# Performance work log

Hardware: AMD Instinct MI355X
Metric: run time of the kernel (lower is better)

The kernel has to match this reference:

```python
import math
import jax, jax.numpy as jnp
import numpy as np

NEG_BIG = -1e12  # matches torch's -1000000000000.0 padding


def setup_inputs() -> dict:
    key = jax.random.key(0)
    k1, k2, k3 = jax.random.split(key, 3)
    bs, n_tok, n_heads, width = 1, 4096, 8, 64
    dst_mxlen, src_mxlen = 32, 64
    q = jax.random.normal(k1, (bs, n_tok, n_heads, width), dtype=jnp.float32)
    k = jax.random.normal(k2, (bs, n_tok, n_heads, width), dtype=jnp.float32)
    v = jax.random.normal(k3, (bs, n_tok, n_heads, width), dtype=jnp.float32)
    # Sliding-window COO: each dst attends to its dst_mxlen preceding tokens (clipped).
    dst = jnp.repeat(jnp.arange(n_tok, dtype=jnp.int32), dst_mxlen)
    cnt = jnp.tile(jnp.arange(dst_mxlen, dtype=jnp.int32), n_tok)
    src = jnp.clip(dst - cnt, 0, n_tok - 1)
    coo = jnp.stack([dst, src, cnt], axis=1)  # [cl, 3]
    return {"v": v, "q": q, "k": k, "coo": coo,
            "dst_mxlen": dst_mxlen, "src_mxlen": src_mxlen, "use_softmax": 1}


def reference(v, q, k, coo, dst_mxlen, src_mxlen, use_softmax):
    bs, n_tok, n_heads, width = q.shape
    cl = coo.shape[0]
    # [b, h, t, w] layout
    qq = jnp.transpose(q, (0, 2, 1, 3))[:, :, coo[:, 0], :]  # [b,h,cl,w]
    kk = jnp.transpose(k, (0, 2, 1, 3))[:, :, coo[:, 1], :]
    vv = jnp.transpose(v, (0, 2, 1, 3))
    scale = -1.0 / math.sqrt(width)
    ww = jnp.sum(jnp.abs(qq - kk), axis=-1) * scale  # [b,h,cl]
    # Padded softmax buffer, last slot is the (optional) softmax denominator pad.
    attn = jnp.full((bs, n_heads, n_tok, dst_mxlen + 1), NEG_BIG, dtype=q.dtype)
    attn = attn.at[:, :, coo[:, 0], coo[:, 2]].set(ww)
    if use_softmax:
        attn = attn.at[:, :, :, -1].set(0.0)
        attn_sm = jax.nn.softmax(attn, axis=-1)
    else:
        attn_sm = jnp.exp(attn)
    attn_sm = attn_sm[:, :, :, :-1]  # [b,h,t,s]
    # Scatter V into the padded buffer: vw[b,h,dst,cnt,:] = vv[b,h,src,:]
    vw = jnp.zeros((bs, n_heads, n_tok, dst_mxlen, width), dtype=q.dtype)
    vw = vw.at[:, :, coo[:, 0], coo[:, 2], :].set(vv[:, :, coo[:, 1], :])
    vo = jnp.einsum('bhds,bhdsw->bdhw', attn_sm, vw)
    return vo
```

## Files before the change

kernel.cpp:

```cpp
#include <hip/hip_runtime.h>
#include <math.h>


typedef float v2f __attribute__((ext_vector_type(2)));

constexpr int H = 8;
constexpr int W = 64;
constexpr int TPW = 2;

template <int CTRL>
__device__ __forceinline__ float dpp_add(float x) {
    int xi = __builtin_bit_cast(int, x);
    int yi = __builtin_amdgcn_update_dpp(0, xi, CTRL, 0xf, 0xf, true);
    return x + __builtin_bit_cast(float, yi);
}

__device__ __forceinline__ float reduce16(float a) {
    a = dpp_add<0xB1>(a);
    a = dpp_add<0x4E>(a);
    a = dpp_add<0x141>(a);
    a = dpp_add<0x140>(a);
    return a;
}

__device__ __forceinline__ float absdiff4(float4 qv, float4 kv) {
    v2f q01 = {qv.x, qv.y}, q23 = {qv.z, qv.w};
    v2f k01 = {kv.x, kv.y}, k23 = {kv.z, kv.w};
    v2f d0 = q01 - k01;
    v2f d1 = q23 - k23;
    v2f a0 = __builtin_elementwise_max(d0, -d0);
    v2f a1 = __builtin_elementwise_max(d1, -d1);
    v2f ss = a0 + a1;
    return ss.x + ss.y;
}

__global__ __launch_bounds__(256) void l1attn_sparse_kernel(
    const float* __restrict__ v,
    const float* __restrict__ q,
    const float* __restrict__ k,
    const int*   __restrict__ p_dst_mxlen,
    const int*   __restrict__ p_use_softmax,
    float*       __restrict__ out,
    int n_tok)
{
    const int dst_mxlen = *p_dst_mxlen;
    const int use_sm    = *p_use_softmax;

    int bid = blockIdx.x;
    if ((gridDim.x & 7) == 0) {
        const int chunk = gridDim.x >> 3;
        bid = (bid & 7) * chunk + (bid >> 3);
    }

    const int sub  = threadIdx.x >> 6;
    const int lane = threadIdx.x & 63;
    const int headhalf = sub >> 1;
    const int winhalf  = sub & 1;

    const int t0 = bid * TPW;
    if (t0 >= n_tok) return;

    const int h     = headhalf * 4 + (lane >> 4);
    const int dbase = (lane & 15) * 4;

    float4 qv[TPW];
    #pragma unroll
    for (int j = 0; j < TPW; ++j) {
        int t = t0 + j; t = t < n_tok ? t : n_tok - 1;
        qv[j] = *reinterpret_cast<const float4*>(q + (t * H + h) * W + dbase);
    }

    v2f   acc01[TPW], acc23[TPW];
    float sump[TPW];
    #pragma unroll
    for (int j = 0; j < TPW; ++j) {
        acc01[j] = (v2f){0.f, 0.f}; acc23[j] = (v2f){0.f, 0.f}; sump[j] = 0.f;
    }

    int s_lo = t0 - (dst_mxlen - 1); s_lo = s_lo < 0 ? 0 : s_lo;
    const int s_hi = (t0 + TPW - 1) < (n_tok - 1) ? (t0 + TPW - 1) : (n_tok - 1);
    const int len  = s_hi - s_lo + 1;
    const int half = (len + 1) >> 1;
    int       my_lo = winhalf ? s_lo + half : s_lo;
    const int my_hi = winhalf ? s_hi       : s_lo + half - 1;

    if (my_lo == 0 && my_hi >= 0) {
        const int base = h * W + dbase;
        const float4 kv = *reinterpret_cast<const float4*>(k + base);
        const float4 vv = *reinterpret_cast<const float4*>(v + base);
        v2f v01 = {vv.x, vv.y}, v23 = {vv.z, vv.w};
        #pragma unroll
        for (int j = 0; j < TPW; ++j) {
            const int t = t0 + j;
            float a = reduce16(absdiff4(qv[j], kv));
            int mm = dst_mxlen - t; mm = mm > 0 ? mm : 0;
            const float p = (float)mm * __expf(a * -0.125f);
            sump[j] += p;
            acc01[j] += p * v01;
            acc23[j] += p * v23;
        }
        my_lo = 1;
    }

    int s = my_lo;
    float4 kc, vc;
    if (s <= my_hi) {
        const int base = (s * H + h) * W + dbase;
        kc = *reinterpret_cast<const float4*>(k + base);
        vc = *reinterpret_cast<const float4*>(v + base);
    }
    for (; s <= my_hi; ++s) {
        const int sn = (s + 1 <= my_hi) ? s + 1 : s;
        const int basen = (sn * H + h) * W + dbase;
        const float4 kn = *reinterpret_cast<const float4*>(k + basen);
        const float4 vn = *reinterpret_cast<const float4*>(v + basen);

        v2f v01 = {vc.x, vc.y}, v23 = {vc.z, vc.w};
        #pragma unroll
        for (int j = 0; j < TPW; ++j) {
            const int t = t0 + j;
            float a = reduce16(absdiff4(qv[j], kc));
            const float m = ((unsigned)(t - s) < (unsigned)dst_mxlen) ? 1.f : 0.f;
            const float p = m * __expf(a * -0.125f);
            sump[j] += p;
            acc01[j] += p * v01;
            acc23[j] += p * v23;
        }
        kc = kn; vc = vn;
    }

    __shared__ float lds[2][TPW][5][64];
    if (winhalf == 1) {
        #pragma unroll
        for (int j = 0; j < TPW; ++j) {
            lds[headhalf][j][0][lane] = acc01[j].x;
            lds[headhalf][j][1][lane] = acc01[j].y;
            lds[headhalf][j][2][lane] = acc23[j].x;
            lds[headhalf][j][3][lane] = acc23[j].y;
            lds[headhalf][j][4][lane] = sump[j];
        }
    }
    __syncthreads();
    if (winhalf == 0) {
        #pragma unroll
        for (int j = 0; j < TPW; ++j) {
            acc01[j].x += lds[headhalf][j][0][lane];
            acc01[j].y += lds[headhalf][j][1][lane];
            acc23[j].x += lds[headhalf][j][2][lane];
            acc23[j].y += lds[headhalf][j][3][lane];
            sump[j]    += lds[headhalf][j][4][lane];

            const int t = t0 + j;
            if (t < n_tok) {
                const float scale = use_sm ? 1.0f / (1.0f + sump[j]) : 1.0f;
                float4 o = {acc01[j].x * scale, acc01[j].y * scale,
                            acc23[j].x * scale, acc23[j].y * scale};
                *reinterpret_cast<float4*>(out + (t * H + h) * W + dbase) = o;
            }
        }
    }
}

extern "C" void kernel_launch(void* const* d_in, const int* in_sizes, int n_in,
                              void* d_out, int out_size, void* d_ws, size_t ws_size,
                              hipStream_t stream) {
    const float* v   = (const float*)d_in[0];
    const float* q   = (const float*)d_in[1];
    const float* k   = (const float*)d_in[2];
    const int*   p_dst_mxlen = (const int*)d_in[4];
    const int*   p_use_sm    = (const int*)d_in[6];
    float* out = (float*)d_out;

    const int n_tok = in_sizes[1] / (H * W);

    const int blocks = (n_tok + TPW - 1) / TPW;
    l1attn_sparse_kernel<<<blocks, 256, 0, stream>>>(
        v, q, k, p_dst_mxlen, p_use_sm, out, n_tok);
}
```

Measured before the change: 21.14 us.

## Give each wave a full source window and batch K/V loads in groups of four

Removes the split of the source window across two waves, along with the shared-memory combine and block barrier. Each wave now handles one token pair and one head half over the whole window, so each block covers two token pairs. K/V rows are loaded in batches of four ahead of compute to expose more memory-level parallelism. The trade-off is a longer serial loop per wave with less parallel work per token, and the batched loads can fetch clamped rows past the window end that are then masked out.

```diff
diff --git a/kernel.cpp b/kernel.cpp
--- a/kernel.cpp
+++ b/kernel.cpp
@@ -4,9 +4,10 @@
 
 typedef float v2f __attribute__((ext_vector_type(2)));
 
-constexpr int H = 8;
-constexpr int W = 64;
+constexpr int H   = 8;
+constexpr int W   = 64;
 constexpr int TPW = 2;
+constexpr int SB  = 4;
 
 template <int CTRL>
 __device__ __forceinline__ float dpp_add(float x) {
@@ -26,8 +27,7 @@
 __device__ __forceinline__ float absdiff4(float4 qv, float4 kv) {
     v2f q01 = {qv.x, qv.y}, q23 = {qv.z, qv.w};
     v2f k01 = {kv.x, kv.y}, k23 = {kv.z, kv.w};
-    v2f d0 = q01 - k01;
-    v2f d1 = q23 - k23;
+    v2f d0 = q01 - k01, d1 = q23 - k23;
     v2f a0 = __builtin_elementwise_max(d0, -d0);
     v2f a1 = __builtin_elementwise_max(d1, -d1);
     v2f ss = a0 + a1;
@@ -52,22 +52,23 @@
         bid = (bid & 7) * chunk + (bid >> 3);
     }
 
-    const int sub  = threadIdx.x >> 6;
+    const int wid  = bid * (blockDim.x >> 6) + (threadIdx.x >> 6);
     const int lane = threadIdx.x & 63;
-    const int headhalf = sub >> 1;
-    const int winhalf  = sub & 1;
 
-    const int t0 = bid * TPW;
+    const int pairIdx = wid >> 1;
+    const int t0 = pairIdx * TPW;
     if (t0 >= n_tok) return;
+    const int hh = wid & 1;
 
-    const int h     = headhalf * 4 + (lane >> 4);
+    const int h     = hh * 4 + (lane >> 4);
     const int dbase = (lane & 15) * 4;
+    const int hoff  = h * W + dbase;
 
     float4 qv[TPW];
     #pragma unroll
     for (int j = 0; j < TPW; ++j) {
         int t = t0 + j; t = t < n_tok ? t : n_tok - 1;
-        qv[j] = *reinterpret_cast<const float4*>(q + (t * H + h) * W + dbase);
+        qv[j] = *reinterpret_cast<const float4*>(q + t * (H * W) + hoff);
     }
 
     v2f   acc01[TPW], acc23[TPW];
@@ -77,17 +78,9 @@
         acc01[j] = (v2f){0.f, 0.f}; acc23[j] = (v2f){0.f, 0.f}; sump[j] = 0.f;
     }
 
-    int s_lo = t0 - (dst_mxlen - 1); s_lo = s_lo < 0 ? 0 : s_lo;
-    const int s_hi = (t0 + TPW - 1) < (n_tok - 1) ? (t0 + TPW - 1) : (n_tok - 1);
-    const int len  = s_hi - s_lo + 1;
-    const int half = (len + 1) >> 1;
-    int       my_lo = winhalf ? s_lo + half : s_lo;
-    const int my_hi = winhalf ? s_hi       : s_lo + half - 1;
-
-    if (my_lo == 0 && my_hi >= 0) {
-        const int base = h * W + dbase;
-        const float4 kv = *reinterpret_cast<const float4*>(k + base);
-        const float4 vv = *reinterpret_cast<const float4*>(v + base);
+    if (t0 - (dst_mxlen - 1) <= 0) {
+        const float4 kv = *reinterpret_cast<const float4*>(k + hoff);
+        const float4 vv = *reinterpret_cast<const float4*>(v + hoff);
         v2f v01 = {vv.x, vv.y}, v23 = {vv.z, vv.w};
         #pragma unroll
         for (int j = 0; j < TPW; ++j) {
@@ -99,64 +92,47 @@
             acc01[j] += p * v01;
             acc23[j] += p * v23;
         }
-        my_lo = 1;
     }
 
-    int s = my_lo;
-    float4 kc, vc;
-    if (s <= my_hi) {
-        const int base = (s * H + h) * W + dbase;
-        kc = *reinterpret_cast<const float4*>(k + base);
-        vc = *reinterpret_cast<const float4*>(v + base);
-    }
-    for (; s <= my_hi; ++s) {
-        const int sn = (s + 1 <= my_hi) ? s + 1 : s;
-        const int basen = (sn * H + h) * W + dbase;
-        const float4 kn = *reinterpret_cast<const float4*>(k + basen);
-        const float4 vn = *reinterpret_cast<const float4*>(v + basen);
+    int s_lo = t0 - (dst_mxlen - 1); s_lo = s_lo < 1 ? 1 : s_lo;
+    int s_hi = t0 + TPW - 1; s_hi = s_hi < n_tok - 1 ? s_hi : n_tok - 1;
 
-        v2f v01 = {vc.x, vc.y}, v23 = {vc.z, vc.w};
+    for (int sbase = s_lo; sbase <= s_hi; sbase += SB) {
+        float4 kb[SB], vb[SB];
         #pragma unroll
-        for (int j = 0; j < TPW; ++j) {
-            const int t = t0 + j;
-            float a = reduce16(absdiff4(qv[j], kc));
-            const float m = ((unsigned)(t - s) < (unsigned)dst_mxlen) ? 1.f : 0.f;
-            const float p = m * __expf(a * -0.125f);
-            sump[j] += p;
-            acc01[j] += p * v01;
-            acc23[j] += p * v23;
+        for (int e = 0; e < SB; ++e) {
+            int su = sbase + e;
+            int sa = su < n_tok ? su : n_tok - 1;
+            const int base = sa * (H * W) + hoff;
+            kb[e] = *reinterpret_cast<const float4*>(k + base);
+            vb[e] = *reinterpret_cast<const float4*>(v + base);
         }
-        kc = kn; vc = vn;
+        #pragma unroll
+        for (int e = 0; e < SB; ++e) {
+            const int su = sbase + e;
+            v2f v01 = {vb[e].x, vb[e].y}, v23 = {vb[e].z, vb[e].w};
+            #pragma unroll
+            for (int j = 0; j < TPW; ++j) {
+                const int t = t0 + j;
+                float a = reduce16(absdiff4(qv[j], kb[e]));
+                const float m =
+                    ((unsigned)(t - su) < (unsigned)dst_mxlen) ? 1.f : 0.f;
+                const float p = m * __expf(a * -0.125f);
+                sump[j] += p;
+                acc01[j] += p * v01;
+                acc23[j] += p * v23;
+            }
+        }
     }
 
-    __shared__ float lds[2][TPW][5][64];
-    if (winhalf == 1) {
-        #pragma unroll
-        for (int j = 0; j < TPW; ++j) {
-            lds[headhalf][j][0][lane] = acc01[j].x;
-            lds[headhalf][j][1][lane] = acc01[j].y;
-            lds[headhalf][j][2][lane] = acc23[j].x;
-            lds[headhalf][j][3][lane] = acc23[j].y;
-            lds[headhalf][j][4][lane] = sump[j];
-        }
-    }
-    __syncthreads();
-    if (winhalf == 0) {
-        #pragma unroll
-        for (int j = 0; j < TPW; ++j) {
-            acc01[j].x += lds[headhalf][j][0][lane];
-            acc01[j].y += lds[headhalf][j][1][lane];
-            acc23[j].x += lds[headhalf][j][2][lane];
-            acc23[j].y += lds[headhalf][j][3][lane];
-            sump[j]    += lds[headhalf][j][4][lane];
-
-            const int t = t0 + j;
-            if (t < n_tok) {
-                const float scale = use_sm ? 1.0f / (1.0f + sump[j]) : 1.0f;
-                float4 o = {acc01[j].x * scale, acc01[j].y * scale,
-                            acc23[j].x * scale, acc23[j].y * scale};
-                *reinterpret_cast<float4*>(out + (t * H + h) * W + dbase) = o;
-            }
+    #pragma unroll
+    for (int j = 0; j < TPW; ++j) {
+        const int t = t0 + j;
+        if (t < n_tok) {
+            const float scale = use_sm ? 1.0f / (1.0f + sump[j]) : 1.0f;
+            float4 o = {acc01[j].x * scale, acc01[j].y * scale,
+                        acc23[j].x * scale, acc23[j].y * scale};
+            *reinterpret_cast<float4*>(out + t * (H * W) + hoff) = o;
         }
     }
 }
@@ -173,7 +149,9 @@
 
     const int n_tok = in_sizes[1] / (H * W);
 
-    const int blocks = (n_tok + TPW - 1) / TPW;
+    const int pairs  = (n_tok + TPW - 1) / TPW;
+    const int waves  = pairs * 2;
+    const int blocks = (waves + 3) / 4;
     l1attn_sparse_kernel<<<blocks, 256, 0, stream>>>(
         v, q, k, p_dst_mxlen, p_use_sm, out, n_tok);
 }
```

New measurement: 22.01 us. 4.1% more time.
